# Kernel tuning notes

Measured on AMD Instinct MI355X. Metric: run time of the kernel, lower is better.

Reference implementation:

```python
import jax, jax.numpy as jnp
import numpy as np

B, S, D, F, E = 8, 1024, 1024, 4096, 8
EPS = 1e-5  # fairseq LayerNorm default


def setup_inputs() -> dict:
    key = jax.random.key(0)
    ks = jax.random.split(key, 4)
    s = 0.02
    return {
        "input_features": jax.random.normal(ks[0], (B, S, D), jnp.float32),
        "centroids": jax.random.normal(ks[1], (E, D), jnp.float32) * 0.1,  # orthogonal_ gain=0.1 stand-in
        "ln_g": jnp.ones((E, D), jnp.float32),
        "ln_b": jnp.zeros((E, D), jnp.float32),
        "w1": jax.random.normal(ks[2], (E, D, F), jnp.float32) * s,
        "b1": jnp.zeros((E, F), jnp.float32),
        "w2": jax.random.normal(ks[3], (E, F, D), jnp.float32) * s,  # torch inits ff2 to zero; random here so bwd is non-trivial
        "b2": jnp.zeros((E, D), jnp.float32),
    }


def reference(input_features, centroids, ln_g, ln_b, w1, b1, w2, b2):
    # Single-worker inference path of BaseLayer: greedy top-1 routing, no shuffle,
    # All2All is the identity. sort_by_expert + per-expert blocks + inverse_sort
    # is equivalent to per-token routing, expressed here with a one-hot combine.
    x = input_features.reshape(-1, D)                         # [T, D] tokens
    aff = jax.lax.stop_gradient(x @ centroids.T)              # [T, E] affinities (torch.no_grad)
    eid = jnp.argmax(aff, axis=-1)                            # [T] greedy_assignment k=1

    # alpha = sigmoid(<token, its expert centroid>) -- grads DO flow to centroids here
    alpha = jax.nn.sigmoid(jnp.sum(x * centroids[eid], axis=-1, keepdims=True))  # [T, 1]

    # Per-expert LayerNorm: normalize once, gather per-token gamma/beta
    mu = jnp.mean(x, axis=-1, keepdims=True)
    var = jnp.mean((x - mu) ** 2, axis=-1, keepdims=True)
    xn = (x - mu) * jax.lax.rsqrt(var + EPS)
    xln = xn * ln_g[eid] + ln_b[eid]                          # [T, D]

    # BaseSublayer: xs + ff2(relu(ff1(LN(xs))))
    # combined with alpha gate: out = alpha*sub(x) + (1-alpha)*x = x + alpha*ffn_residual
    onehot = jax.nn.one_hot(eid, E, dtype=x.dtype)            # [T, E] dispatch mask
    ffn = jnp.zeros_like(x)
    for e in range(E):  # small fixed expert loop (structurally distinct weights)
        h = jax.nn.relu(xln @ w1[e] + b1[e])                  # [T, F]
        ffn = ffn + onehot[:, e:e + 1] * (h @ w2[e] + b2[e])  # [T, D]

    out = x + alpha * ffn
    return out.reshape(input_features.shape)
```

## Files before the change

kernel.cpp:

```cpp
#include <hip/hip_runtime.h>

#define NT 8192
#define DIM 1024
#define FDIM 4096
#define NEXP 8

typedef __attribute__((ext_vector_type(8))) short bfx8;
typedef __attribute__((ext_vector_type(4))) float fx4;

__device__ __forceinline__ unsigned short f2bf(float f) {
  union { float f; unsigned u; } v; v.f = f;
  unsigned u = v.u;
  unsigned r = u + 0x7FFFu + ((u >> 16) & 1u);
  return (unsigned short)(r >> 16);
}

__device__ __forceinline__ void gload16(const void* g, void* l) {
  __builtin_amdgcn_global_load_lds(
      (const __attribute__((address_space(1))) unsigned int*)g,
      (__attribute__((address_space(3))) unsigned int*)l, 16, 0, 0);
}

__global__ void k_zero(int* __restrict__ counts) {
  if (threadIdx.x < NEXP) counts[threadIdx.x] = 0;
}

__device__ __forceinline__ void tr_tile(
    const float* __restrict__ src, unsigned short* __restrict__ dst,
    int R, int C, int r0, int c0, float* T, int t)
{
  const int lane = t & 63, wv = t >> 6;
  const int rsub = wv * 2 + (lane >> 5);
  const int cb = (lane & 31) ^ rsub;
#pragma unroll
  for (int i = 0; i < 8; ++i) {
    const int rbase = i * 8 + wv * 2;
    gload16(src + (size_t)(r0 + rbase + (lane >> 5)) * C + c0 + cb * 4,
            &T[rbase * 128]);
  }
  __syncthreads();
#pragma unroll
  for (int it = 0; it < 4; ++it) {
    const int c = (t >> 3) + it * 32, q = t & 7;
    unsigned short o[8];
#pragma unroll
    for (int u = 0; u < 8; ++u)
      o[u] = f2bf(T[(q * 8 + u) * 128 + ((((c >> 2) ^ u) << 2) | (c & 3))]);
    *(uint4*)(dst + (size_t)(c0 + c) * R + r0 + q * 8) = *(const uint4*)o;
  }
}

__global__ __launch_bounds__(256) void k_fused(
    const float* __restrict__ x, const float* __restrict__ cent,
    const float* __restrict__ g, const float* __restrict__ b,
    const float* __restrict__ w1, const float* __restrict__ w2,
    int* __restrict__ eid, float* __restrict__ alpha, int* __restrict__ counts,
    unsigned short* __restrict__ xln,
    unsigned short* __restrict__ w1t, unsigned short* __restrict__ w2t)
{
  __shared__ float T[64 * 128];
  __shared__ float part[4][NEXP], ps[4], pss[4];
  __shared__ float sMu, sRstd;
  __shared__ int sE;
  const int bid = blockIdx.x, tid = threadIdx.x;

  if (bid < NT) {
    const int t = bid;
    const float4 xv = ((const float4*)(x + (size_t)t * DIM))[tid];
    float acc[NEXP];
#pragma unroll
    for (int e = 0; e < NEXP; ++e) {
      const float4 cv = ((const float4*)(cent + (size_t)e * DIM))[tid];
      acc[e] = xv.x * cv.x + xv.y * cv.y + xv.z * cv.z + xv.w * cv.w;
    }
    float s = xv.x + xv.y + xv.z + xv.w;
    float ss = xv.x * xv.x + xv.y * xv.y + xv.z * xv.z + xv.w * xv.w;
#pragma unroll
    for (int off = 32; off > 0; off >>= 1) {
#pragma unroll
      for (int e = 0; e < NEXP; ++e) acc[e] += __shfl_down(acc[e], off);
      s += __shfl_down(s, off); ss += __shfl_down(ss, off);
    }
    const int lane = tid & 63, w = tid >> 6;
    if (lane == 0) {
#pragma unroll
      for (int e = 0; e < NEXP; ++e) part[w][e] = acc[e];
      ps[w] = s; pss[w] = ss;
    }
    __syncthreads();
    if (tid == 0) {
      int best = 0; float bv = -1e30f;
#pragma unroll
      for (int e = 0; e < NEXP; ++e) {
        float v = part[0][e] + part[1][e] + part[2][e] + part[3][e];
        if (v > bv) { bv = v; best = e; }
      }
      eid[t] = best;
      alpha[t] = 1.0f / (1.0f + expf(-bv));
      atomicAdd(&counts[best], 1);
      const float sum = ps[0] + ps[1] + ps[2] + ps[3];
      const float sq  = pss[0] + pss[1] + pss[2] + pss[3];
      const float mu = sum * (1.0f / DIM);
      const float var = sq * (1.0f / DIM) - mu * mu;
      sE = best; sMu = mu; sRstd = rsqrtf(var + 1e-5f);
    }
    __syncthreads();
    const int e = sE;
    const float mu = sMu, rstd = sRstd;
    const float4 gv = ((const float4*)(g + (size_t)e * DIM))[tid];
    const float4 bv4 = ((const float4*)(b + (size_t)e * DIM))[tid];
    ushort4 o;
    o.x = f2bf((xv.x - mu) * rstd * gv.x + bv4.x);
    o.y = f2bf((xv.y - mu) * rstd * gv.y + bv4.y);
    o.z = f2bf((xv.z - mu) * rstd * gv.z + bv4.z);
    o.w = f2bf((xv.w - mu) * rstd * gv.w + bv4.w);
    ((ushort4*)(xln + (size_t)t * DIM))[tid] = o;
  } else if (bid < NT + 4096) {
    const int i = bid - NT;
    const int e = i >> 9, rem = i & 511;
    tr_tile(w1 + (size_t)e * DIM * FDIM, w1t + (size_t)e * DIM * FDIM,
            DIM, FDIM, (rem & 15) * 64, (rem >> 4) * 128, T, tid);
  } else {
    const int i = bid - NT - 4096;
    const int e = i >> 9, rem = i & 511;
    tr_tile(w2 + (size_t)e * FDIM * DIM, w2t + (size_t)e * FDIM * DIM,
            FDIM, DIM, (rem >> 3) * 64, (rem & 7) * 128, T, tid);
  }
}

__global__ void k_scan(const int* __restrict__ counts, int* __restrict__ bs, int* __restrict__ cur) {
  if (threadIdx.x == 0) {
    int s = 0;
    for (int e = 0; e < NEXP; ++e) { bs[e] = s; cur[e] = s; s += counts[e]; }
  }
}

__global__ void k_rowtok(const int* __restrict__ eid, int* __restrict__ cur,
                         int* __restrict__ row_tok) {
  const int t = blockIdx.x * 256 + threadIdx.x;
  const int e = eid[t];
  const int pos = atomicAdd(&cur[e], 1);
  row_tok[pos] = t;
}

template<int K, int N, bool FIRST>
__global__ __launch_bounds__(256) void k_gemm(
    const unsigned short* __restrict__ A,
    const unsigned short* __restrict__ Bt,
    const float* __restrict__ bias,
    const int* __restrict__ bs, const int* __restrict__ counts,
    unsigned short* __restrict__ Hout,
    const int* __restrict__ row_tok, const float* __restrict__ alpha,
    const float* __restrict__ xin, float* __restrict__ out)
{
  const int MB = NT / 128;
  const int bid = blockIdx.x;
  const int e = bid & 7;
  const int l = bid >> 3;
  const int m0 = (l % MB) * 128;
  const int cnt = counts[e];
  if (m0 >= cnt) return;
  const int n0 = (l / MB) * 128;
  const int rbase = bs[e];

  __shared__ __align__(16) char smem[32 * 132 * 4];
  unsigned short* lA = (unsigned short*)smem;
  unsigned short* lB = (unsigned short*)(smem + 8192);
  float* Lf = (float*)smem;

  const int tid = threadIdx.x;
  const int lane = tid & 63, wv = tid >> 6;
  const int wm = (wv >> 1) * 64, wn = (wv & 1) * 64;
  const int lr = lane & 15, lg = lane >> 4;

  fx4 acc[4][4] = {};

  const unsigned short* Bte = Bt + (size_t)e * N * K;

  const unsigned short* aP[2];
  const unsigned short* bP[2];
#pragma unroll
  for (int p = 0; p < 2; ++p) {
    const int g = p * 256 + tid;
    const int row = g >> 2, kq = (g & 3) * 8;
    int ar = rbase + m0 + row;
    ar = ar < NT ? ar : NT - 1;
    if constexpr (FIRST) {
      const int tok = row_tok[ar];
      aP[p] = A + (size_t)tok * K + kq;
    } else {
      aP[p] = A + (size_t)ar * K + kq;
    }
    bP[p] = Bte + (size_t)(n0 + row) * K + kq;
  }

  for (int k0 = 0; k0 < K; k0 += 32) {
    gload16(aP[0] + k0, &lA[(0 * 4 + wv) * 512]);
    gload16(aP[1] + k0, &lA[(1 * 4 + wv) * 512]);
    gload16(bP[0] + k0, &lB[(0 * 4 + wv) * 512]);
    gload16(bP[1] + k0, &lB[(1 * 4 + wv) * 512]);
    __syncthreads();
    bfx8 bf[4];
#pragma unroll
    for (int j = 0; j < 4; ++j)
      bf[j] = *(const bfx8*)(&lB[(wn + j * 16 + lr) * 32 + lg * 8]);
#pragma unroll
    for (int i = 0; i < 4; ++i) {
      const bfx8 af = *(const bfx8*)(&lA[(wm + i * 16 + lr) * 32 + lg * 8]);
#pragma unroll
      for (int j = 0; j < 4; ++j)
        acc[i][j] = __builtin_amdgcn_mfma_f32_16x16x32_bf16(af, bf[j], acc[i][j], 0, 0, 0);
    }
    __syncthreads();
  }

  const float* be = bias + (size_t)e * N;
  float bcol[4];
#pragma unroll
  for (int j = 0; j < 4; ++j) bcol[j] = be[n0 + wn + j * 16 + lr];

#pragma unroll
  for (int i = 0; i < 4; ++i) {
    __syncthreads();
#pragma unroll
    for (int r2 = 0; r2 < 4; ++r2) {
      const int rowp = (wv >> 1) * 16 + lg * 4 + r2;
#pragma unroll
      for (int j = 0; j < 4; ++j) {
        float v = acc[i][j][r2] + bcol[j];
        if (FIRST) v = v > 0.f ? v : 0.f;
        Lf[rowp * 132 + wn + j * 16 + lr] = v;
      }
    }
    __syncthreads();
    if constexpr (FIRST) {
#pragma unroll
      for (int s = 0; s < 2; ++s) {
        const int tsk = tid + 256 * s;
        const int rr = tsk >> 4, cg = tsk & 15;
        const int ra = i * 16 + ((rr >> 4) << 6) + (rr & 15);
        if (m0 + ra < cnt) {
          const float4 a = *(const float4*)&Lf[rr * 132 + cg * 8];
          const float4 b = *(const float4*)&Lf[rr * 132 + cg * 8 + 4];
          unsigned short o[8] = { f2bf(a.x), f2bf(a.y), f2bf(a.z), f2bf(a.w),
                                  f2bf(b.x), f2bf(b.y), f2bf(b.z), f2bf(b.w) };
          *(uint4*)(Hout + (size_t)(rbase + m0 + ra) * N + n0 + cg * 8) =
              *(const uint4*)o;
        }
      }
    } else {
#pragma unroll
      for (int s = 0; s < 4; ++s) {
        const int tsk = tid + 256 * s;
        const int rr = tsk >> 5, c4 = tsk & 31;
        const int ra = i * 16 + ((rr >> 4) << 6) + (rr & 15);
        if (m0 + ra < cnt) {
          const int tok = row_tok[rbase + m0 + ra];
          const float al = alpha[tok];
          const float4 v = *(const float4*)&Lf[rr * 132 + c4 * 4];
          const float4 xr = *(const float4*)(xin + (size_t)tok * N + n0 + c4 * 4);
          float4 o;
          o.x = xr.x + al * v.x;
          o.y = xr.y + al * v.y;
          o.z = xr.z + al * v.z;
          o.w = xr.w + al * v.w;
          *(float4*)(out + (size_t)tok * N + n0 + c4 * 4) = o;
        }
      }
    }
  }
}

extern "C" void kernel_launch(void* const* d_in, const int* in_sizes, int n_in,
                              void* d_out, int out_size, void* d_ws, size_t ws_size,
                              hipStream_t stream)
{
  const float* x    = (const float*)d_in[0];
  const float* cent = (const float*)d_in[1];
  const float* ln_g = (const float*)d_in[2];
  const float* ln_b = (const float*)d_in[3];
  const float* w1   = (const float*)d_in[4];
  const float* b1   = (const float*)d_in[5];
  const float* w2   = (const float*)d_in[6];
  const float* b2   = (const float*)d_in[7];
  float* out = (float*)d_out;

  char* ws = (char*)d_ws;
  unsigned short* xln  = (unsigned short*)(ws);
  unsigned short* hbuf = (unsigned short*)(ws + (16ull << 20));
  unsigned short* w1t  = (unsigned short*)(ws + (80ull << 20));
  unsigned short* w2t  = (unsigned short*)(ws + (144ull << 20));
  char* tail = ws + (208ull << 20);
  int*    eid    = (int*)(tail);
  float*  alpha  = (float*)(tail + 32768);
  int*    rowtok = (int*)(tail + 65536);
  int*    counts = (int*)(tail + 98304);
  int*    basep  = counts + 16;
  int*    cur    = counts + 32;

  k_zero<<<1, 64, 0, stream>>>(counts);
  k_fused<<<NT + 8192, 256, 0, stream>>>(
      x, cent, ln_g, ln_b, w1, w2, eid, alpha, counts, xln, w1t, w2t);
  k_scan<<<1, 1, 0, stream>>>(counts, basep, cur);
  k_rowtok<<<NT / 256, 256, 0, stream>>>(eid, cur, rowtok);
  k_gemm<DIM, FDIM, true><<<NEXP * (NT / 128) * (FDIM / 128), 256, 0, stream>>>(
      xln, w1t, b1, basep, counts, hbuf, rowtok, nullptr, nullptr, nullptr);
  k_gemm<FDIM, DIM, false><<<NEXP * (NT / 128) * (DIM / 128), 256, 0, stream>>>(
      hbuf, w2t, b2, basep, counts, nullptr, rowtok, alpha, x, out);
}
```

Baseline: 442.0 us.

## Enlarge first expert GEMM tile to 256x256 with 512 threads and direct stores

The first expert GEMM is split into its own kernel with 256x256 output tiles and 8 waves per block, which roughly halves the global and LDS traffic per MFMA for the W1 projection. Its epilogue now writes bf16 values straight from registers with scalar 2-byte stores instead of staging through LDS, giving up coalesced 16-byte stores. The weight transpose thread mapping is also changed so that consecutive lanes handle consecutive columns. The larger tiles raise register pressure (32 accumulator vectors per wave) and can waste more work on partially filled expert tiles.

```diff
diff --git a/kernel.cpp b/kernel.cpp
--- a/kernel.cpp
+++ b/kernel.cpp
@@ -23,31 +23,6 @@
 
 __global__ void k_zero(int* __restrict__ counts) {
   if (threadIdx.x < NEXP) counts[threadIdx.x] = 0;
-}
-
-__device__ __forceinline__ void tr_tile(
-    const float* __restrict__ src, unsigned short* __restrict__ dst,
-    int R, int C, int r0, int c0, float* T, int t)
-{
-  const int lane = t & 63, wv = t >> 6;
-  const int rsub = wv * 2 + (lane >> 5);
-  const int cb = (lane & 31) ^ rsub;
-#pragma unroll
-  for (int i = 0; i < 8; ++i) {
-    const int rbase = i * 8 + wv * 2;
-    gload16(src + (size_t)(r0 + rbase + (lane >> 5)) * C + c0 + cb * 4,
-            &T[rbase * 128]);
-  }
-  __syncthreads();
-#pragma unroll
-  for (int it = 0; it < 4; ++it) {
-    const int c = (t >> 3) + it * 32, q = t & 7;
-    unsigned short o[8];
-#pragma unroll
-    for (int u = 0; u < 8; ++u)
-      o[u] = f2bf(T[(q * 8 + u) * 128 + ((((c >> 2) ^ u) << 2) | (c & 3))]);
-    *(uint4*)(dst + (size_t)(c0 + c) * R + r0 + q * 8) = *(const uint4*)o;
-  }
 }
 
 __global__ __launch_bounds__(256) void k_fused(
@@ -115,16 +90,41 @@
     o.z = f2bf((xv.z - mu) * rstd * gv.z + bv4.z);
     o.w = f2bf((xv.w - mu) * rstd * gv.w + bv4.w);
     ((ushort4*)(xln + (size_t)t * DIM))[tid] = o;
-  } else if (bid < NT + 4096) {
-    const int i = bid - NT;
-    const int e = i >> 9, rem = i & 511;
-    tr_tile(w1 + (size_t)e * DIM * FDIM, w1t + (size_t)e * DIM * FDIM,
-            DIM, FDIM, (rem & 15) * 64, (rem >> 4) * 128, T, tid);
   } else {
-    const int i = bid - NT - 4096;
-    const int e = i >> 9, rem = i & 511;
-    tr_tile(w2 + (size_t)e * FDIM * DIM, w2t + (size_t)e * FDIM * DIM,
-            FDIM, DIM, (rem >> 3) * 64, (rem & 7) * 128, T, tid);
+    const float* src;
+    unsigned short* dst;
+    int R, C, r0, c0;
+    if (bid < NT + 4096) {
+      const int i = bid - NT, e = i >> 9, rem = i & 511;
+      R = DIM; C = FDIM;
+      src = w1 + (size_t)e * DIM * FDIM; dst = w1t + (size_t)e * DIM * FDIM;
+      r0 = (rem & 15) * 64; c0 = (rem >> 4) * 128;
+    } else {
+      const int i = bid - NT - 4096, e = i >> 9, rem = i & 511;
+      R = FDIM; C = DIM;
+      src = w2 + (size_t)e * FDIM * DIM; dst = w2t + (size_t)e * FDIM * DIM;
+      r0 = (rem >> 3) * 64; c0 = (rem & 7) * 128;
+    }
+    const int lane = tid & 63, wv = tid >> 6;
+    const int rsub = wv * 2 + (lane >> 5);
+    const int cb = (lane & 31) ^ rsub;
+#pragma unroll
+    for (int i = 0; i < 8; ++i) {
+      const int rbase = i * 8 + wv * 2;
+      gload16(src + (size_t)(r0 + rbase + (lane >> 5)) * C + c0 + cb * 4,
+              &T[rbase * 128]);
+    }
+    __syncthreads();
+    const int q = tid >> 5, cbase = tid & 31;
+#pragma unroll
+    for (int it = 0; it < 4; ++it) {
+      const int c = cbase + it * 32;
+      unsigned short o[8];
+#pragma unroll
+      for (int u = 0; u < 8; ++u)
+        o[u] = f2bf(T[(q * 8 + u) * 128 + ((((c >> 2) ^ u) << 2) | (c & 3))]);
+      *(uint4*)(dst + (size_t)(c0 + c) * R + r0 + q * 8) = *(const uint4*)o;
+    }
   }
 }
 
@@ -143,13 +143,96 @@
   row_tok[pos] = t;
 }
 
-template<int K, int N, bool FIRST>
-__global__ __launch_bounds__(256) void k_gemm(
+__global__ __launch_bounds__(512) void k_gemm1(
     const unsigned short* __restrict__ A,
     const unsigned short* __restrict__ Bt,
     const float* __restrict__ bias,
     const int* __restrict__ bs, const int* __restrict__ counts,
     unsigned short* __restrict__ Hout,
+    const int* __restrict__ row_tok)
+{
+  const int MB = NT / 256;
+  const int bid = blockIdx.x;
+  const int e = bid & 7;
+  const int l = bid >> 3;
+  const int m0 = (l % MB) * 256;
+  const int cnt = counts[e];
+  if (m0 >= cnt) return;
+  const int n0 = (l / MB) * 256;
+  const int rbase = bs[e];
+
+  __shared__ unsigned short lA[256 * 32];
+  __shared__ unsigned short lB[256 * 32];
+
+  const int tid = threadIdx.x;
+  const int lane = tid & 63, wv = tid >> 6;
+  const int wm = (wv >> 2) * 128, wn = (wv & 3) * 64;
+  const int lr = lane & 15, lg = lane >> 4;
+
+  fx4 acc[8][4] = {};
+
+  const unsigned short* Bte = Bt + (size_t)e * FDIM * DIM;
+
+  const unsigned short* aP[2];
+  const unsigned short* bP[2];
+#pragma unroll
+  for (int p = 0; p < 2; ++p) {
+    const int g = p * 512 + tid;
+    const int row = g >> 2, kq = (g & 3) * 8;
+    int ar = rbase + m0 + row;
+    ar = ar < NT ? ar : NT - 1;
+    const int tok = row_tok[ar];
+    aP[p] = A + (size_t)tok * DIM + kq;
+    bP[p] = Bte + (size_t)(n0 + row) * DIM + kq;
+  }
+
+  for (int k0 = 0; k0 < DIM; k0 += 32) {
+    gload16(aP[0] + k0, &lA[(0 * 8 + wv) * 512]);
+    gload16(aP[1] + k0, &lA[(1 * 8 + wv) * 512]);
+    gload16(bP[0] + k0, &lB[(0 * 8 + wv) * 512]);
+    gload16(bP[1] + k0, &lB[(1 * 8 + wv) * 512]);
+    __syncthreads();
+    bfx8 bf[4];
+#pragma unroll
+    for (int j = 0; j < 4; ++j)
+      bf[j] = *(const bfx8*)(&lB[(wn + j * 16 + lr) * 32 + lg * 8]);
+#pragma unroll
+    for (int i = 0; i < 8; ++i) {
+      const bfx8 af = *(const bfx8*)(&lA[(wm + i * 16 + lr) * 32 + lg * 8]);
+#pragma unroll
+      for (int j = 0; j < 4; ++j)
+        acc[i][j] = __builtin_amdgcn_mfma_f32_16x16x32_bf16(af, bf[j], acc[i][j], 0, 0, 0);
+    }
+    __syncthreads();
+  }
+
+  const float* be = bias + (size_t)e * FDIM;
+  float bcol[4];
+#pragma unroll
+  for (int j = 0; j < 4; ++j) bcol[j] = be[n0 + wn + j * 16 + lr];
+
+#pragma unroll
+  for (int i = 0; i < 8; ++i) {
+#pragma unroll
+    for (int r2 = 0; r2 < 4; ++r2) {
+      const int rl = wm + i * 16 + lg * 4 + r2;
+      if (m0 + rl >= cnt) continue;
+      unsigned short* hrow = Hout + (size_t)(rbase + m0 + rl) * FDIM;
+#pragma unroll
+      for (int j = 0; j < 4; ++j) {
+        const int col = n0 + wn + j * 16 + lr;
+        float v = acc[i][j][r2] + bcol[j];
+        hrow[col] = f2bf(v > 0.f ? v : 0.f);
+      }
+    }
+  }
+}
+
+__global__ __launch_bounds__(256) void k_gemm2(
+    const unsigned short* __restrict__ A,
+    const unsigned short* __restrict__ Bt,
+    const float* __restrict__ bias,
+    const int* __restrict__ bs, const int* __restrict__ counts,
     const int* __restrict__ row_tok, const float* __restrict__ alpha,
     const float* __restrict__ xin, float* __restrict__ out)
 {
@@ -175,7 +258,7 @@
 
   fx4 acc[4][4] = {};
 
-  const unsigned short* Bte = Bt + (size_t)e * N * K;
+  const unsigned short* Bte = Bt + (size_t)e * DIM * FDIM;
 
   const unsigned short* aP[2];
   const unsigned short* bP[2];
@@ -185,16 +268,11 @@
     const int row = g >> 2, kq = (g & 3) * 8;
     int ar = rbase + m0 + row;
     ar = ar < NT ? ar : NT - 1;
-    if constexpr (FIRST) {
-      const int tok = row_tok[ar];
-      aP[p] = A + (size_t)tok * K + kq;
-    } else {
-      aP[p] = A + (size_t)ar * K + kq;
-    }
-    bP[p] = Bte + (size_t)(n0 + row) * K + kq;
-  }
-
-  for (int k0 = 0; k0 < K; k0 += 32) {
+    aP[p] = A + (size_t)ar * FDIM + kq;
+    bP[p] = Bte + (size_t)(n0 + row) * FDIM + kq;
+  }
+
+  for (int k0 = 0; k0 < FDIM; k0 += 32) {
     gload16(aP[0] + k0, &lA[(0 * 4 + wv) * 512]);
     gload16(aP[1] + k0, &lA[(1 * 4 + wv) * 512]);
     gload16(bP[0] + k0, &lB[(0 * 4 + wv) * 512]);
@@ -214,7 +292,7 @@
     __syncthreads();
   }
 
-  const float* be = bias + (size_t)e * N;
+  const float* be = bias + (size_t)e * DIM;
   float bcol[4];
 #pragma unroll
   for (int j = 0; j < 4; ++j) bcol[j] = be[n0 + wn + j * 16 + lr];
@@ -226,46 +304,26 @@
     for (int r2 = 0; r2 < 4; ++r2) {
       const int rowp = (wv >> 1) * 16 + lg * 4 + r2;
 #pragma unroll
-      for (int j = 0; j < 4; ++j) {
-        float v = acc[i][j][r2] + bcol[j];
-        if (FIRST) v = v > 0.f ? v : 0.f;
-        Lf[rowp * 132 + wn + j * 16 + lr] = v;
-      }
-    }
-    __syncthreads();
-    if constexpr (FIRST) {
-#pragma unroll
-      for (int s = 0; s < 2; ++s) {
-        const int tsk = tid + 256 * s;
-        const int rr = tsk >> 4, cg = tsk & 15;
-        const int ra = i * 16 + ((rr >> 4) << 6) + (rr & 15);
-        if (m0 + ra < cnt) {
-          const float4 a = *(const float4*)&Lf[rr * 132 + cg * 8];
-          const float4 b = *(const float4*)&Lf[rr * 132 + cg * 8 + 4];
-          unsigned short o[8] = { f2bf(a.x), f2bf(a.y), f2bf(a.z), f2bf(a.w),
-                                  f2bf(b.x), f2bf(b.y), f2bf(b.z), f2bf(b.w) };
-          *(uint4*)(Hout + (size_t)(rbase + m0 + ra) * N + n0 + cg * 8) =
-              *(const uint4*)o;
-        }
-      }
-    } else {
-#pragma unroll
-      for (int s = 0; s < 4; ++s) {
-        const int tsk = tid + 256 * s;
-        const int rr = tsk >> 5, c4 = tsk & 31;
-        const int ra = i * 16 + ((rr >> 4) << 6) + (rr & 15);
-        if (m0 + ra < cnt) {
-          const int tok = row_tok[rbase + m0 + ra];
-          const float al = alpha[tok];
-          const float4 v = *(const float4*)&Lf[rr * 132 + c4 * 4];
-          const float4 xr = *(const float4*)(xin + (size_t)tok * N + n0 + c4 * 4);
-          float4 o;
-          o.x = xr.x + al * v.x;
-          o.y = xr.y + al * v.y;
-          o.z = xr.z + al * v.z;
-          o.w = xr.w + al * v.w;
-          *(float4*)(out + (size_t)tok * N + n0 + c4 * 4) = o;
-        }
+      for (int j = 0; j < 4; ++j)
+        Lf[rowp * 132 + wn + j * 16 + lr] = acc[i][j][r2] + bcol[j];
+    }
+    __syncthreads();
+#pragma unroll
+    for (int s = 0; s < 4; ++s) {
+      const int tsk = tid + 256 * s;
+      const int rr = tsk >> 5, c4 = tsk & 31;
+      const int ra = i * 16 + ((rr >> 4) << 6) + (rr & 15);
+      if (m0 + ra < cnt) {
+        const int tok = row_tok[rbase + m0 + ra];
+        const float al = alpha[tok];
+        const float4 v = *(const float4*)&Lf[rr * 132 + c4 * 4];
+        const float4 xr = *(const float4*)(xin + (size_t)tok * DIM + n0 + c4 * 4);
+        float4 o;
+        o.x = xr.x + al * v.x;
+        o.y = xr.y + al * v.y;
+        o.z = xr.z + al * v.z;
+        o.w = xr.w + al * v.w;
+        *(float4*)(out + (size_t)tok * DIM + n0 + c4 * 4) = o;
       }
     }
   }
@@ -303,8 +361,8 @@
       x, cent, ln_g, ln_b, w1, w2, eid, alpha, counts, xln, w1t, w2t);
   k_scan<<<1, 1, 0, stream>>>(counts, basep, cur);
   k_rowtok<<<NT / 256, 256, 0, stream>>>(eid, cur, rowtok);
-  k_gemm<DIM, FDIM, true><<<NEXP * (NT / 128) * (FDIM / 128), 256, 0, stream>>>(
-      xln, w1t, b1, basep, counts, hbuf, rowtok, nullptr, nullptr, nullptr);
-  k_gemm<FDIM, DIM, false><<<NEXP * (NT / 128) * (DIM / 128), 256, 0, stream>>>(
-      hbuf, w2t, b2, basep, counts, nullptr, rowtok, alpha, x, out);
-}
+  k_gemm1<<<NEXP * (NT / 256) * (FDIM / 256), 512, 0, stream>>>(
+      xln, w1t, b1, basep, counts, hbuf, rowtok);
+  k_gemm2<<<NEXP * (NT / 128) * (DIM / 128), 256, 0, stream>>>(
+      hbuf, w2t, b2, basep, counts, rowtok, alpha, x, out);
+}
```

After: 527.4 us. 19.3% more time.
